# Optimization experiments

Measured on AMD Instinct MI355X. Metric: run time of the kernel, lower is better.

The kernel has to match this reference:

```python
import jax, jax.numpy as jnp
import numpy as np

B, T, D_IN, D_OUT, H = 4, 2048, 768, 768, 12
HD = D_OUT // H  # 64


def setup_inputs() -> dict:
    key = jax.random.key(0)
    ks = jax.random.split(key, 6)
    s_in = 1.0 / np.sqrt(D_IN)
    s_out = 1.0 / np.sqrt(D_OUT)
    return {
        "x": jax.random.normal(ks[0], (B, T, D_IN), dtype=jnp.float32),
        "Wq": jax.random.uniform(ks[1], (D_IN, D_OUT), jnp.float32, -s_in, s_in),
        "Wk": jax.random.uniform(ks[2], (D_IN, D_OUT), jnp.float32, -s_in, s_in),
        "Wv": jax.random.uniform(ks[3], (D_IN, D_OUT), jnp.float32, -s_in, s_in),
        "Wo": jax.random.uniform(ks[4], (D_OUT, D_OUT), jnp.float32, -s_out, s_out),
        "bo": jax.random.uniform(ks[5], (D_OUT,), jnp.float32, -s_out, s_out),
    }


def reference(x, Wq, Wk, Wv, Wo, bo):
    b, t, _ = x.shape
    # QKV projections (no bias, per qkv_bias=False), split into heads: [b,h,t,hd]
    q = (x @ Wq).reshape(b, t, H, HD).transpose(0, 2, 1, 3)
    k = (x @ Wk).reshape(b, t, H, HD).transpose(0, 2, 1, 3)
    v = (x @ Wv).reshape(b, t, H, HD).transpose(0, 2, 1, 3)
    # NOTE: original calls masked_fill (non-in-place) and discards the result,
    # so NO causal mask is actually applied. Faithfully reproduce that.
    scores = jnp.einsum("bhqd,bhkd->bhqk", q, k)  # [b,h,t,t]
    attn = jax.nn.softmax(scores / jnp.sqrt(jnp.float32(HD)), axis=-1)
    # dropout p=0.0 (eval) -> identity
    ctx = jnp.einsum("bhqk,bhkd->bhqd", attn, v)  # [b,h,t,hd]
    ctx = ctx.transpose(0, 2, 1, 3).reshape(b, t, D_OUT)
    return ctx @ Wo + bo
```

## Files before the change

### kernel.cpp

```cpp
#include <hip/hip_runtime.h>
#include <hip/hip_bf16.h>
#include <stdint.h>


#define HH   12
#define TT   2048
#define DIN  768
#define DOUT 768
#define HD   64
#define BB   4
#define MTOT (BB*TT)
#define NQKV (3*DOUT)
#define QSCALE 0.1803368801111832f

typedef float  float4v  __attribute__((ext_vector_type(4)));
typedef float  float16v __attribute__((ext_vector_type(16)));
typedef __bf16 bf16x8   __attribute__((ext_vector_type(8)));
typedef short  short8v  __attribute__((ext_vector_type(8)));

#define AS1 __attribute__((address_space(1)))
#define AS3 __attribute__((address_space(3)))

static __device__ __forceinline__ void gload_lds16(const void* g, void* l) {
    __builtin_amdgcn_global_load_lds((AS1 void*)g, (AS3 void*)l, 16, 0, 0);
}

static __device__ __forceinline__ short f2bf(float f) {
    __bf16 h = (__bf16)f;
    return __builtin_bit_cast(short, h);
}

__global__ __launch_bounds__(256) void cast_x_kernel(const float* __restrict__ x,
                                                     short* __restrict__ xb, int n4) {
    int i = blockIdx.x * 256 + threadIdx.x;
    if (i >= n4) return;
    float4 v = ((const float4*)x)[i];
    short4 o;
    o.x = f2bf(v.x); o.y = f2bf(v.y); o.z = f2bf(v.z); o.w = f2bf(v.w);
    ((short4*)xb)[i] = o;
}

__global__ __launch_bounds__(256) void prep_w_kernel(const float* __restrict__ Wq,
                                                     const float* __restrict__ Wk,
                                                     const float* __restrict__ Wv,
                                                     const float* __restrict__ Wo,
                                                     short* __restrict__ Wqkvt,
                                                     short* __restrict__ Wot) {
    __shared__ short tile[32 * 33];
    const int bx = blockIdx.x, by = blockIdx.y, bz = blockIdx.z;
    const float* W = (bz == 0) ? Wq : (bz == 1) ? Wk : (bz == 2) ? Wv : Wo;
    const int tx = threadIdx.x & 31, ty = threadIdx.x >> 5;
    for (int i = 0; i < 4; i++) {
        int k = by * 32 + ty + i * 8;
        tile[(ty + i * 8) * 33 + tx] = f2bf(W[(size_t)k * DOUT + bx * 32 + tx]);
    }
    __syncthreads();
    for (int i = 0; i < 4; i++) {
        int n = bx * 32 + ty + i * 8;
        int k = by * 32 + tx;
        short v = tile[tx * 33 + ty + i * 8];
        if (bz < 3) Wqkvt[(size_t)(bz * DOUT + n) * DIN + k] = v;
        else        Wot[(size_t)n * DOUT + k] = v;
    }
}

__global__ __launch_bounds__(256) void qkv_gemm_kernel(const short* __restrict__ Xb,
                                                       const short* __restrict__ Wt,
                                                       short* __restrict__ Qb,
                                                       short* __restrict__ Kb,
                                                       short* __restrict__ Vt) {
    __shared__ __align__(16) short lds[16384];
    short* ldsA = lds;
    short* ldsB = lds + 4096;
    const int t = threadIdx.x;
    const int w = t >> 6, lane = t & 63;
    const int quad = lane >> 4, l15 = lane & 15;
    const int m0 = blockIdx.x * 128, n0 = blockIdx.y * 128;
    const int wm = (w >> 1) * 64, wn = (w & 1) * 64;

    float4v acc[4][4];
    for (int i = 0; i < 4; i++)
        for (int j = 0; j < 4; j++)
            acc[i][j] = (float4v)0.0f;

    const int rA = t >> 2;
    const int cSw = ((t & 3) ^ ((t >> 3) & 3)) * 8;
    const short* gA0 = Xb + (size_t)(m0 + rA) * DIN + cSw;
    const short* gB0 = Wt + (size_t)(n0 + rA) * DIN + cSw;
    const int pos = (quad ^ ((l15 >> 1) & 3)) * 8;

    for (int k0 = 0; k0 < DIN; k0 += 32) {
        gload_lds16(gA0 + k0,            &ldsA[t * 8]);
        gload_lds16(gA0 + 64 * DIN + k0, &ldsA[(t + 256) * 8]);
        gload_lds16(gB0 + k0,            &ldsB[t * 8]);
        gload_lds16(gB0 + 64 * DIN + k0, &ldsB[(t + 256) * 8]);
        __syncthreads();
        bf16x8 af[4], bfr[4];
        for (int i = 0; i < 4; i++) af[i]  = *(const bf16x8*)&ldsA[(wm + i * 16 + l15) * 32 + pos];
        for (int j = 0; j < 4; j++) bfr[j] = *(const bf16x8*)&ldsB[(wn + j * 16 + l15) * 32 + pos];
        for (int i = 0; i < 4; i++)
            for (int j = 0; j < 4; j++)
                acc[i][j] = __builtin_amdgcn_mfma_f32_16x16x32_bf16(af[i], bfr[j], acc[i][j], 0, 0, 0);
        __syncthreads();
    }

    const int which = n0 / DOUT;
    if (which < 2) {
        short* ldsT = lds;
        const float sc = (which == 0) ? QSCALE : 1.0f;
        short* dst = (which == 0) ? Qb : Kb;
        const int n0sec = n0 - which * DOUT;
        for (int i = 0; i < 4; i++)
            for (int j = 0; j < 4; j++) {
                int col = wn + j * 16 + l15;
                int cx = col >> 3, co = col & 7;
                for (int r = 0; r < 4; r++) {
                    int row = wm + i * 16 + quad * 4 + r;
                    ldsT[row * 128 + ((cx ^ (row & 7)) * 8 + co)] = f2bf(acc[i][j][r] * sc);
                }
            }
        __syncthreads();
        for (int p = 0; p < 8; p++) {
            int row = p * 16 + (t >> 4);
            int cL = t & 15;
            short8v v = *(const short8v*)&ldsT[row * 128 + ((cL ^ (row & 7)) * 8)];
            int mg = m0 + row;
            int b2 = mg >> 11, tq = mg & 2047;
            int colg = n0sec + cL * 8;
            int hh = colg >> 6, d = colg & 63;
            *(short8v*)&dst[((size_t)((b2 * HH + hh) * TT + tq) << 6) + d] = v;
        }
    } else {
        short* ldsT = lds;
        const int n0r = n0 - 2 * DOUT;
        const int b = m0 >> 11, tq0 = m0 & 2047;
        for (int i = 0; i < 4; i++)
            for (int j = 0; j < 4; j++)
                for (int r = 0; r < 4; r++) {
                    int nl = wn + j * 16 + l15;
                    int ml = wm + i * 16 + quad * 4 + r;
                    int c = ml >> 3, o = ml & 7;
                    ldsT[nl * 128 + ((c ^ (nl & 7)) * 8 + o)] = f2bf(acc[i][j][r]);
                }
        __syncthreads();
        for (int p = 0; p < 8; p++) {
            int nrow = p * 16 + (t >> 4);
            int cc = t & 15;
            short8v v = *(const short8v*)&ldsT[nrow * 128 + ((cc ^ (nrow & 7)) * 8)];
            int colg = n0r + nrow;
            int hh = colg >> 6, d = colg & 63;
            *(short8v*)&Vt[(size_t)((b * HH + hh) * HD + d) * TT + tq0 + cc * 8] = v;
        }
    }
}

__global__ __launch_bounds__(256, 3) void attn_kernel(const short* __restrict__ Qb,
                                                      const short* __restrict__ Kb,
                                                      const short* __restrict__ Vt,
                                                      short* __restrict__ Ctx) {
    __shared__ __align__(16) short ldsK[2][64 * 64];
    __shared__ __align__(16) short ldsV[2][64 * 64];
    const int t = threadIdx.x;
    const int w = t >> 6, lane = t & 63;
    const int half = lane >> 5, m = lane & 31;
    const int bh = blockIdx.x;
    const int b = bh / HH, h = bh - b * HH;
    const int q0 = blockIdx.y * 128 + w * 32;

    const short* Qbase = Qb + (size_t)bh * TT * HD;
    const short* Kbase = Kb + (size_t)bh * TT * HD;
    const short* Vbase = Vt + (size_t)bh * HD * TT;

    bf16x8 qf[4];
#pragma unroll
    for (int s = 0; s < 4; s++)
        qf[s] = *(const bf16x8*)&Qbase[(q0 + m) * HD + s * 16 + half * 8];

    int kOff[2], vOff[2];
    {
        int r5 = t >> 3;
        int pi = ((r5 >> 3) & 1) * 16 + ((r5 >> 2) & 1) * 8 + ((r5 >> 4) & 1) * 4 + (r5 & 3);
#pragma unroll
        for (int g = 0; g < 2; g++) {
            kOff[g] = (g * 32 + pi) * 64 + (((t & 7) ^ (r5 & 7)) * 8);
            int vrow = g * 32 + r5;
            vOff[g] = vrow * TT + (((t & 7) ^ (vrow & 7)) * 8);
        }
    }

    auto stage = [&](int buf, int u0) {
#pragma unroll
        for (int g = 0; g < 2; g++)
            gload_lds16(Kbase + (size_t)u0 * 64 + kOff[g], &ldsK[buf][(g * 256 + t) * 8]);
#pragma unroll
        for (int g = 0; g < 2; g++)
            gload_lds16(Vbase + (size_t)u0 + vOff[g], &ldsV[buf][(g * 256 + t) * 8]);
    };

    float16v accO[2];
    accO[0] = (float16v)0.0f;
    accO[1] = (float16v)0.0f;
    float lsum = 0.0f;

    stage(0, 0);

    for (int it = 0; it < TT / 64; ++it) {
        __syncthreads();
        const int buf = it & 1;
        if (it + 1 < TT / 64) stage(buf ^ 1, (it + 1) * 64);
        const short* K_ = &ldsK[buf][0];
        const short* V_ = &ldsV[buf][0];

#pragma unroll
        for (int kt = 0; kt < 2; kt++) {
            float16v st = (float16v)0.0f;
#pragma unroll
            for (int s = 0; s < 4; s++) {
                bf16x8 ka = *(const bf16x8*)&K_[(kt * 32 + m) * 64 + (((s * 2 + half) ^ (m & 7)) * 8)];
                st = __builtin_amdgcn_mfma_f32_32x32x16_bf16(ka, qf[s], st, 0, 0, 0);
            }
            float pe[16];
#pragma unroll
            for (int i = 0; i < 16; i++) pe[i] = __builtin_amdgcn_exp2f(st[i]);
            float s01 = 0.0f;
#pragma unroll
            for (int i = 0; i < 16; i++) s01 += pe[i];
            lsum += s01;
            bf16x8 ap[2];
#pragma unroll
            for (int i = 0; i < 4; i++) {
                ap[0][i]     = (__bf16)pe[i];
                ap[0][4 + i] = (__bf16)pe[8 + i];
                ap[1][i]     = (__bf16)pe[4 + i];
                ap[1][4 + i] = (__bf16)pe[12 + i];
            }
#pragma unroll
            for (int ks = 0; ks < 2; ks++)
#pragma unroll
                for (int dt = 0; dt < 2; dt++) {
                    int row = dt * 32 + m;
                    bf16x8 bv = *(const bf16x8*)&V_[row * 64 + (((kt * 4 + ks * 2 + half) ^ (row & 7)) * 8)];
                    accO[dt] = __builtin_amdgcn_mfma_f32_32x32x16_bf16(ap[ks], bv, accO[dt], 0, 0, 0);
                }
        }
    }

    {
        float v = lsum + __shfl_xor(lsum, 32);
        float linv = 1.0f / v;
#pragma unroll
        for (int s = 0; s < 4; s++)
#pragma unroll
            for (int i = 0; i < 4; i++) {
                int reg = s * 4 + i;
                int qrow = i + s * 8 + half * 4;
                float ln = __shfl(linv, qrow);
                int qg = q0 + qrow;
                size_t base = (size_t)(b * TT + qg) * DOUT + h * HD + m;
                Ctx[base]      = f2bf(accO[0][reg] * ln);
                Ctx[base + 32] = f2bf(accO[1][reg] * ln);
            }
    }
}

__global__ __launch_bounds__(256) void out_gemm_kernel(const short* __restrict__ Cb,
                                                       const short* __restrict__ Wot,
                                                       const float* __restrict__ bo,
                                                       float* __restrict__ out) {
    __shared__ __align__(16) short ldsA[64 * 32];
    __shared__ __align__(16) short ldsB[128 * 32];
    const int t = threadIdx.x;
    const int w = t >> 6, lane = t & 63;
    const int quad = lane >> 4, l15 = lane & 15;
    const int m0 = blockIdx.x * 64, n0 = blockIdx.y * 128;
    const int wn = w * 32;

    float4v acc[4][2];
    for (int i = 0; i < 4; i++)
        for (int j = 0; j < 2; j++)
            acc[i][j] = (float4v)0.0f;

    const int rA = t >> 2;
    const int cSw = ((t & 3) ^ ((t >> 3) & 3)) * 8;
    const short* gA0 = Cb + (size_t)(m0 + rA) * DOUT + cSw;
    const short* gB0 = Wot + (size_t)(n0 + rA) * DOUT + cSw;
    const int pos = (quad ^ ((l15 >> 1) & 3)) * 8;

    for (int k0 = 0; k0 < DOUT; k0 += 32) {
        gload_lds16(gA0 + k0,             &ldsA[t * 8]);
        gload_lds16(gB0 + k0,             &ldsB[t * 8]);
        gload_lds16(gB0 + 64 * DOUT + k0, &ldsB[(t + 256) * 8]);
        __syncthreads();
        bf16x8 af[4], bfr[2];
        for (int i = 0; i < 4; i++) af[i]  = *(const bf16x8*)&ldsA[(i * 16 + l15) * 32 + pos];
        for (int j = 0; j < 2; j++) bfr[j] = *(const bf16x8*)&ldsB[(wn + j * 16 + l15) * 32 + pos];
        for (int i = 0; i < 4; i++)
            for (int j = 0; j < 2; j++)
                acc[i][j] = __builtin_amdgcn_mfma_f32_16x16x32_bf16(af[i], bfr[j], acc[i][j], 0, 0, 0);
        __syncthreads();
    }

    for (int i = 0; i < 4; i++) {
        int m = m0 + i * 16 + quad * 4;
        for (int j = 0; j < 2; j++) {
            int n = n0 + wn + j * 16 + l15;
            float bias = bo[n];
            for (int r = 0; r < 4; r++)
                out[(size_t)(m + r) * DOUT + n] = acc[i][j][r] + bias;
        }
    }
}

extern "C" void kernel_launch(void* const* d_in, const int* in_sizes, int n_in,
                              void* d_out, int out_size, void* d_ws, size_t ws_size,
                              hipStream_t stream) {
    const float* x  = (const float*)d_in[0];
    const float* Wq = (const float*)d_in[1];
    const float* Wk = (const float*)d_in[2];
    const float* Wv = (const float*)d_in[3];
    const float* Wo = (const float*)d_in[4];
    const float* bo = (const float*)d_in[5];
    float* out = (float*)d_out;

    char* ws = (char*)d_ws;
    short* Xb    = (short*)(ws + 0);
    short* Wqkvt = (short*)(ws + 12582912);
    short* Wot   = (short*)(ws + 16121856);
    short* Qb    = (short*)(ws + 17301504);
    short* Kb    = (short*)(ws + 29884416);
    short* Vt    = (short*)(ws + 42467328);
    short* Cb    = (short*)(ws + 55050240);

    cast_x_kernel<<<(MTOT * DIN / 4 + 255) / 256, 256, 0, stream>>>(x, Xb, MTOT * DIN / 4);
    prep_w_kernel<<<dim3(24, 24, 4), 256, 0, stream>>>(Wq, Wk, Wv, Wo, Wqkvt, Wot);
    qkv_gemm_kernel<<<dim3(MTOT / 128, NQKV / 128), 256, 0, stream>>>(Xb, Wqkvt, Qb, Kb, Vt);
    attn_kernel<<<dim3(BB * HH, TT / 128), 256, 0, stream>>>(Qb, Kb, Vt, Cb);
    out_gemm_kernel<<<dim3(MTOT / 64, DOUT / 128), 256, 0, stream>>>(Cb, Wot, bo, out);
}
```

Baseline: 208.2 us.

## Merge x cast into weight prep kernel and double GEMM K-step to 64

Folds the x fp32-to-bf16 cast into the weight transpose kernel as an extra grid slice (bz==4) with a grid-stride loop, saving one kernel launch. Both the QKV and output GEMMs now stage 64-wide K tiles in LDS with an 8-chunk XOR swizzle and issue two MFMA sub-steps per tile. This halves the number of barrier pairs per GEMM. It raises LDS use per block, which may cut occupancy. The cast slice now runs on only 576 blocks, so it gets less parallelism than before.

```diff
diff --git a/kernel.cpp b/kernel.cpp
--- a/kernel.cpp
+++ b/kernel.cpp
@@ -30,24 +30,27 @@
     return __builtin_bit_cast(short, h);
 }
 
-__global__ __launch_bounds__(256) void cast_x_kernel(const float* __restrict__ x,
-                                                     short* __restrict__ xb, int n4) {
-    int i = blockIdx.x * 256 + threadIdx.x;
-    if (i >= n4) return;
-    float4 v = ((const float4*)x)[i];
-    short4 o;
-    o.x = f2bf(v.x); o.y = f2bf(v.y); o.z = f2bf(v.z); o.w = f2bf(v.w);
-    ((short4*)xb)[i] = o;
-}
-
-__global__ __launch_bounds__(256) void prep_w_kernel(const float* __restrict__ Wq,
-                                                     const float* __restrict__ Wk,
-                                                     const float* __restrict__ Wv,
-                                                     const float* __restrict__ Wo,
-                                                     short* __restrict__ Wqkvt,
-                                                     short* __restrict__ Wot) {
+__global__ __launch_bounds__(256) void prep_kernel(const float* __restrict__ x,
+                                                   const float* __restrict__ Wq,
+                                                   const float* __restrict__ Wk,
+                                                   const float* __restrict__ Wv,
+                                                   const float* __restrict__ Wo,
+                                                   short* __restrict__ Xb,
+                                                   short* __restrict__ Wqkvt,
+                                                   short* __restrict__ Wot) {
     __shared__ short tile[32 * 33];
     const int bx = blockIdx.x, by = blockIdx.y, bz = blockIdx.z;
+    if (bz == 4) {
+        const int n4 = MTOT * DIN / 4;
+        const int base = (by * 24 + bx) * 256 + threadIdx.x;
+        for (int i = base; i < n4; i += 24 * 24 * 256) {
+            float4 v = ((const float4*)x)[i];
+            short4 o;
+            o.x = f2bf(v.x); o.y = f2bf(v.y); o.z = f2bf(v.z); o.w = f2bf(v.w);
+            ((short4*)Xb)[i] = o;
+        }
+        return;
+    }
     const float* W = (bz == 0) ? Wq : (bz == 1) ? Wk : (bz == 2) ? Wv : Wo;
     const int tx = threadIdx.x & 31, ty = threadIdx.x >> 5;
     for (int i = 0; i < 4; i++) {
@@ -71,7 +74,7 @@
                                                        short* __restrict__ Vt) {
     __shared__ __align__(16) short lds[16384];
     short* ldsA = lds;
-    short* ldsB = lds + 4096;
+    short* ldsB = lds + 8192;
     const int t = threadIdx.x;
     const int w = t >> 6, lane = t & 63;
     const int quad = lane >> 4, l15 = lane & 15;
@@ -83,26 +86,43 @@
         for (int j = 0; j < 4; j++)
             acc[i][j] = (float4v)0.0f;
 
-    const int rA = t >> 2;
-    const int cSw = ((t & 3) ^ ((t >> 3) & 3)) * 8;
-    const short* gA0 = Xb + (size_t)(m0 + rA) * DIN + cSw;
-    const short* gB0 = Wt + (size_t)(n0 + rA) * DIN + cSw;
-    const int pos = (quad ^ ((l15 >> 1) & 3)) * 8;
-
-    for (int k0 = 0; k0 < DIN; k0 += 32) {
-        gload_lds16(gA0 + k0,            &ldsA[t * 8]);
-        gload_lds16(gA0 + 64 * DIN + k0, &ldsA[(t + 256) * 8]);
-        gload_lds16(gB0 + k0,            &ldsB[t * 8]);
-        gload_lds16(gB0 + 64 * DIN + k0, &ldsB[(t + 256) * 8]);
-        __syncthreads();
-        bf16x8 af[4], bfr[4];
-        for (int i = 0; i < 4; i++) af[i]  = *(const bf16x8*)&ldsA[(wm + i * 16 + l15) * 32 + pos];
-        for (int j = 0; j < 4; j++) bfr[j] = *(const bf16x8*)&ldsB[(wn + j * 16 + l15) * 32 + pos];
-        for (int i = 0; i < 4; i++)
-            for (int j = 0; j < 4; j++)
-                acc[i][j] = __builtin_amdgcn_mfma_f32_16x16x32_bf16(af[i], bfr[j], acc[i][j], 0, 0, 0);
-        __syncthreads();
-    }
+    int sOff[4];
+    int sRow[4];
+#pragma unroll
+    for (int g = 0; g < 4; g++) {
+        int slot = g * 256 + t;
+        int row = slot >> 3, ch = slot & 7;
+        sRow[g] = row;
+        sOff[g] = ((ch ^ (row & 7)) * 8);
+    }
+    const int pos_r = 0;
+
+    for (int k0 = 0; k0 < DIN; k0 += 64) {
+#pragma unroll
+        for (int g = 0; g < 4; g++)
+            gload_lds16(Xb + (size_t)(m0 + sRow[g]) * DIN + k0 + sOff[g], &ldsA[(g * 256 + t) * 8]);
+#pragma unroll
+        for (int g = 0; g < 4; g++)
+            gload_lds16(Wt + (size_t)(n0 + sRow[g]) * DIN + k0 + sOff[g], &ldsB[(g * 256 + t) * 8]);
+        __syncthreads();
+#pragma unroll
+        for (int f = 0; f < 2; f++) {
+            bf16x8 af[4], bfr[4];
+            for (int i = 0; i < 4; i++) {
+                int row = wm + i * 16 + l15;
+                af[i] = *(const bf16x8*)&ldsA[row * 64 + (((f * 4 + quad) ^ (row & 7)) * 8)];
+            }
+            for (int j = 0; j < 4; j++) {
+                int row = wn + j * 16 + l15;
+                bfr[j] = *(const bf16x8*)&ldsB[row * 64 + (((f * 4 + quad) ^ (row & 7)) * 8)];
+            }
+            for (int i = 0; i < 4; i++)
+                for (int j = 0; j < 4; j++)
+                    acc[i][j] = __builtin_amdgcn_mfma_f32_16x16x32_bf16(af[i], bfr[j], acc[i][j], 0, 0, 0);
+        }
+        __syncthreads();
+    }
+    (void)pos_r;
 
     const int which = n0 / DOUT;
     if (which < 2) {
@@ -267,8 +287,8 @@
                                                        const short* __restrict__ Wot,
                                                        const float* __restrict__ bo,
                                                        float* __restrict__ out) {
-    __shared__ __align__(16) short ldsA[64 * 32];
-    __shared__ __align__(16) short ldsB[128 * 32];
+    __shared__ __align__(16) short ldsA[64 * 64];
+    __shared__ __align__(16) short ldsB[128 * 64];
     const int t = threadIdx.x;
     const int w = t >> 6, lane = t & 63;
     const int quad = lane >> 4, l15 = lane & 15;
@@ -280,23 +300,37 @@
         for (int j = 0; j < 2; j++)
             acc[i][j] = (float4v)0.0f;
 
-    const int rA = t >> 2;
-    const int cSw = ((t & 3) ^ ((t >> 3) & 3)) * 8;
-    const short* gA0 = Cb + (size_t)(m0 + rA) * DOUT + cSw;
-    const short* gB0 = Wot + (size_t)(n0 + rA) * DOUT + cSw;
-    const int pos = (quad ^ ((l15 >> 1) & 3)) * 8;
-
-    for (int k0 = 0; k0 < DOUT; k0 += 32) {
-        gload_lds16(gA0 + k0,             &ldsA[t * 8]);
-        gload_lds16(gB0 + k0,             &ldsB[t * 8]);
-        gload_lds16(gB0 + 64 * DOUT + k0, &ldsB[(t + 256) * 8]);
-        __syncthreads();
-        bf16x8 af[4], bfr[2];
-        for (int i = 0; i < 4; i++) af[i]  = *(const bf16x8*)&ldsA[(i * 16 + l15) * 32 + pos];
-        for (int j = 0; j < 2; j++) bfr[j] = *(const bf16x8*)&ldsB[(wn + j * 16 + l15) * 32 + pos];
-        for (int i = 0; i < 4; i++)
-            for (int j = 0; j < 2; j++)
-                acc[i][j] = __builtin_amdgcn_mfma_f32_16x16x32_bf16(af[i], bfr[j], acc[i][j], 0, 0, 0);
+    for (int k0 = 0; k0 < DOUT; k0 += 64) {
+#pragma unroll
+        for (int g = 0; g < 2; g++) {
+            int slot = g * 256 + t;
+            int row = slot >> 3, ch = slot & 7;
+            gload_lds16(Cb + (size_t)(m0 + row) * DOUT + k0 + ((ch ^ (row & 7)) * 8),
+                        &ldsA[slot * 8]);
+        }
+#pragma unroll
+        for (int g = 0; g < 4; g++) {
+            int slot = g * 256 + t;
+            int row = slot >> 3, ch = slot & 7;
+            gload_lds16(Wot + (size_t)(n0 + row) * DOUT + k0 + ((ch ^ (row & 7)) * 8),
+                        &ldsB[slot * 8]);
+        }
+        __syncthreads();
+#pragma unroll
+        for (int f = 0; f < 2; f++) {
+            bf16x8 af[4], bfr[2];
+            for (int i = 0; i < 4; i++) {
+                int row = i * 16 + l15;
+                af[i] = *(const bf16x8*)&ldsA[row * 64 + (((f * 4 + quad) ^ (row & 7)) * 8)];
+            }
+            for (int j = 0; j < 2; j++) {
+                int row = wn + j * 16 + l15;
+                bfr[j] = *(const bf16x8*)&ldsB[row * 64 + (((f * 4 + quad) ^ (row & 7)) * 8)];
+            }
+            for (int i = 0; i < 4; i++)
+                for (int j = 0; j < 2; j++)
+                    acc[i][j] = __builtin_amdgcn_mfma_f32_16x16x32_bf16(af[i], bfr[j], acc[i][j], 0, 0, 0);
+        }
         __syncthreads();
     }
 
@@ -331,8 +365,7 @@
     short* Vt    = (short*)(ws + 42467328);
     short* Cb    = (short*)(ws + 55050240);
 
-    cast_x_kernel<<<(MTOT * DIN / 4 + 255) / 256, 256, 0, stream>>>(x, Xb, MTOT * DIN / 4);
-    prep_w_kernel<<<dim3(24, 24, 4), 256, 0, stream>>>(Wq, Wk, Wv, Wo, Wqkvt, Wot);
+    prep_kernel<<<dim3(24, 24, 5), 256, 0, stream>>>(x, Wq, Wk, Wv, Wo, Xb, Wqkvt, Wot);
     qkv_gemm_kernel<<<dim3(MTOT / 128, NQKV / 128), 256, 0, stream>>>(Xb, Wqkvt, Qb, Kb, Vt);
     attn_kernel<<<dim3(BB * HH, TT / 128), 256, 0, stream>>>(Qb, Kb, Vt, Cb);
     out_gemm_kernel<<<dim3(MTOT / 64, DOUT / 128), 256, 0, stream>>>(Cb, Wot, bo, out);
```

Result: no change. 211.0 us (+1.3%).
